# Kernel tuning notes

Measured on AMD Instinct MI355X. Metric: run time of the kernel, lower is better.

Reference implementation:

```python
import jax, jax.numpy as jnp
import numpy as np

H_IMG, W_IMG = 2160, 3840


def _avgpool3x3(x):
    # AvgPool2d(3, stride=1, padding=1), count_include_pad=True -> divide by 9 always
    s = jax.lax.reduce_window(x, 0.0, jax.lax.add, (3, 3, 1), (1, 1, 1), 'SAME')
    return s / 9.0


def setup_inputs() -> dict:
    key = jax.random.key(0)
    k1, k2, k3, k4 = jax.random.split(key, 4)
    depth = jax.random.uniform(k1, (H_IMG, W_IMG), jnp.float32) * 4.0 + 0.5
    rgb = jax.random.uniform(k2, (H_IMG, W_IMG, 3), jnp.float32)
    mask = jax.random.randint(k3, (H_IMG, W_IMG), 0, 2, jnp.int32)
    l = jax.random.normal(k4, (9, 3), jnp.float32) * 0.3
    fx = fy = 3000.0
    cx, cy = W_IMG / 2.0, H_IMG / 2.0
    CameraParam = jnp.array([[fx, 0.0, cx], [0.0, fy, cy], [0.0, 0.0, 1.0]], jnp.float32)
    return {'depth': depth, 'rgb': rgb, 'mask': mask, 'l': l, 'CameraParam': CameraParam}


def reference(depth, rgb, mask, l, CameraParam):
    nrows, ncols = depth.shape
    imask = mask > 0                      # [H, W] bool
    m3 = imask[..., None]                 # [H, W, 1]

    # Homogeneous pixel grid -> back-projected rays (precomputed in torch __init__)
    yy, xx = jnp.meshgrid(jnp.arange(nrows, dtype=jnp.float32),
                          jnp.arange(ncols, dtype=jnp.float32), indexing='ij')
    p2d = jnp.stack([xx, yy, jnp.ones_like(xx)], axis=-1)      # [H, W, 3]
    Kinv = jnp.linalg.inv(CameraParam)
    p3d = jnp.einsum('ij,hwj->hwi', Kinv, p2d)                 # [H, W, 3]

    # Depth -> 3D points, shifted neighbors (zero-padded at borders)
    p = p3d * depth[..., None]                                 # [H, W, 3]
    pl = jnp.pad(p[:, 1:, :], ((0, 0), (0, 1), (0, 0)))        # right neighbor
    pu = jnp.pad(p[1:, :, :], ((0, 1), (0, 0), (0, 0)))        # down neighbor

    n = jnp.cross(pl - p, pu - p)                              # [H, W, 3]
    norm = jnp.linalg.norm(n, axis=-1, keepdims=True)
    n = n / jnp.maximum(norm, 1e-12)                           # F.normalize

    nx, ny, nz = n[..., 0], n[..., 1], n[..., 2]
    ones = jnp.ones_like(nx)
    Hsh = jnp.stack([ones, ny, nz, nx, nx * ny, ny * nz,
                     -nx * nx - ny * ny + 2.0 * nz * nz,
                     nz * nx, nx * nx - ny * ny], axis=-1)     # [H, W, 9]
    B = jnp.einsum('hwk,kc->hwc', Hsh, l)                      # [H, W, 3]

    # Scatter into full image: zero outside mask (matches render_img[imask] = B)
    render = jnp.where(m3, B, 0.0)
    render_mean = jax.lax.stop_gradient(_avgpool3x3(render))   # render_img.detach()
    rgbmean = _avgpool3x3(jax.lax.stop_gradient(rgb))          # rgb.detach()

    diff = (render - render_mean) - (rgb - rgbmean)
    cnt = jnp.sum(imask).astype(jnp.float32) * 3.0             # MSE over masked elems
    loss = jnp.sum(jnp.where(m3, diff * diff, 0.0)) / cnt
    return loss
```

## Files before the change

### kernel.cpp

```cpp
#include <hip/hip_runtime.h>
#include <math.h>

#define H_IMG 2160
#define W_IMG 3840
#define SPAN 252
#define NSX 16
#define HS 12
#define WPB 4
#define NSY 45
#define NBLOCKS (NSX * NSY)
#define NBINS 2048

__global__ __launch_bounds__(256, 3) void shading_main(
    const float* __restrict__ depth,
    const float* __restrict__ rgb,
    const int*   __restrict__ mask,
    const float* __restrict__ lmat,
    const float* __restrict__ K,
    float* __restrict__ accum,
    int direct)
{
    const int tid  = threadIdx.x;
    const int lane = tid & 63;
    const int wv   = tid >> 6;
    const int sx   = blockIdx.x;
    const int x0   = sx * SPAN;
    const int y0   = blockIdx.y * (WPB * HS) + wv * HS;
    const int colBase = x0 + 4 * lane;
    const bool fullIn = (colBase + 3) < W_IMG;

    const float m00 = K[0], m01 = K[1], m02 = K[2];
    const float m10 = K[3], m11 = K[4], m12 = K[5];
    const float m20 = K[6], m21 = K[7], m22 = K[8];
    const float det = m00*(m11*m22 - m12*m21)
                    - m01*(m10*m22 - m12*m20)
                    + m02*(m10*m21 - m11*m20);
    const float id  = 1.0f / det;
    const float i00 = (m11*m22 - m12*m21) * id;
    const float i01 = (m02*m21 - m01*m22) * id;
    const float i02 = (m01*m12 - m02*m11) * id;
    const float i10 = (m12*m20 - m10*m22) * id;
    const float i11 = (m00*m22 - m02*m20) * id;
    const float i12 = (m02*m10 - m00*m12) * id;
    const float i20 = (m10*m21 - m11*m20) * id;
    const float i21 = (m01*m20 - m00*m21) * id;
    const float i22 = (m00*m11 - m01*m10) * id;

    float L[27];
    #pragma unroll
    for (int i = 0; i < 27; ++i) L[i] = lmat[i];

    float wout[4];
    #pragma unroll
    for (int k = 0; k < 4; ++k) {
        const int c  = colBase + k;
        const int lc = 4 * lane + k;
        const bool v = (c < W_IMG) && (lc <= SPAN) && (lc >= 1 || sx == 0);
        wout[k] = v ? 1.0f : 0.0f;
    }
    const float qm1s = (lane == 0) ? 0.0f : 1.0f;

    float rx = fmaf(i00, (float)colBase, fmaf(i01, (float)(y0 - 1), i02));
    float ry = fmaf(i10, (float)colBase, fmaf(i11, (float)(y0 - 1), i12));
    float rz = fmaf(i20, (float)colBase, fmaf(i21, (float)(y0 - 1), i22));

    const float4 Z4 = make_float4(0.f, 0.f, 0.f, 0.f);

    float4 dC = Z4, dN = Z4;
    float4 raC = Z4, rbC = Z4, rcC = Z4;
    int4   mC  = make_int4(0, 0, 0, 0);
    if (fullIn) {
        if (y0 > 0) {
            const long pix = (long)(y0 - 1) * W_IMG + colBase;
            dC  = *(const float4*)(depth + pix);
            raC = *(const float4*)(rgb + pix * 3);
            rbC = *(const float4*)(rgb + pix * 3 + 4);
            rcC = *(const float4*)(rgb + pix * 3 + 8);
            mC  = *(const int4*)(mask + pix);
        }
        dN = *(const float4*)(depth + (long)y0 * W_IMG + colBase);
    }

    float sA0[4] = {0,0,0,0}, sA1[4] = {0,0,0,0}, sA2[4] = {0,0,0,0};
    float sB0[4] = {0,0,0,0}, sB1[4] = {0,0,0,0}, sB2[4] = {0,0,0,0};
    float qB0[4] = {0,0,0,0}, qB1[4] = {0,0,0,0}, qB2[4] = {0,0,0,0};
    float wB[4]  = {0,0,0,0};
    float accS = 0.f, accC = 0.f;

    #pragma unroll 1
    for (int j = 0; j < HS + 2; ++j) {
        const int h = y0 - 1 + j;

        float4 dP = Z4, raN = Z4, rbN = Z4, rcN = Z4;
        int4   mN = make_int4(0, 0, 0, 0);
        if (fullIn) {
            if (h + 2 < H_IMG)
                dP = *(const float4*)(depth + (long)(h + 2) * W_IMG + colBase);
            if (h + 1 < H_IMG) {
                const long pix = (long)(h + 1) * W_IMG + colBase;
                raN = *(const float4*)(rgb + pix * 3);
                rbN = *(const float4*)(rgb + pix * 3 + 4);
                rcN = *(const float4*)(rgb + pix * 3 + 8);
                mN  = *(const int4*)(mask + pix);
            }
        }

        const float dcv[4] = {dC.x, dC.y, dC.z, dC.w};
        const float dnv[4] = {dN.x, dN.y, dN.z, dN.w};
        const float rrv[12] = {raC.x, raC.y, raC.z, raC.w,
                               rbC.x, rbC.y, rbC.z, rbC.w,
                               rcC.x, rcC.y, rcC.z, rcC.w};
        const int   mmv[4] = {mC.x, mC.y, mC.z, mC.w};
        const float dcR = __shfl_down(dC.x, 1, 64);

        float qC0[4], qC1[4], qC2[4], wC[4];
        float rxk = rx, ryk = ry, rzk = rz;
        #pragma unroll
        for (int k = 0; k < 4; ++k) {
            const float d0 = dcv[k];
            const float dR = (k < 3) ? dcv[k + 1] : dcR;
            const float dD = dnv[k];
            const float px = rxk * d0, py = ryk * d0, pz = rzk * d0;
            const float ax = (rxk + i00) * dR - px;
            const float ay = (ryk + i10) * dR - py;
            const float az = (rzk + i20) * dR - pz;
            const float bx = (rxk + i01) * dD - px;
            const float by = (ryk + i11) * dD - py;
            const float bz = (rzk + i21) * dD - pz;
            float nx = ay*bz - az*by;
            float ny = az*bx - ax*bz;
            float nz = ax*by - ay*bx;
            const float nn  = nx*nx + ny*ny + nz*nz;
            const float inr = __builtin_amdgcn_rsqf(fmaxf(nn, 1e-24f));
            nx *= inr; ny *= inr; nz *= inr;
            const float h4 = nx*ny, h5 = ny*nz, h7 = nz*nx;
            const float nx2 = nx*nx, ny2 = ny*ny, nz2 = nz*nz;
            const float h6 = 2.f*nz2 - nx2 - ny2;
            const float h8 = nx2 - ny2;
            const float B0 = L[0] + ny*L[3] + nz*L[6] + nx*L[9]  + h4*L[12] + h5*L[15] + h6*L[18] + h7*L[21] + h8*L[24];
            const float B1 = L[1] + ny*L[4] + nz*L[7] + nx*L[10] + h4*L[13] + h5*L[16] + h6*L[19] + h7*L[22] + h8*L[25];
            const float B2 = L[2] + ny*L[5] + nz*L[8] + nx*L[11] + h4*L[14] + h5*L[17] + h6*L[20] + h7*L[23] + h8*L[26];
            const float m  = (mmv[k] > 0) ? 1.0f : 0.0f;
            qC0[k] = fmaf(m, B0, -rrv[3*k + 0]);
            qC1[k] = fmaf(m, B1, -rrv[3*k + 1]);
            qC2[k] = fmaf(m, B2, -rrv[3*k + 2]);
            wC[k]  = m * wout[k];
            rxk += i00; ryk += i10; rzk += i20;
        }

        float sC0[4], sC1[4], sC2[4];
        {
            const float a0 = __shfl_up(qC0[3], 1, 64) * qm1s;
            const float a1 = __shfl_up(qC1[3], 1, 64) * qm1s;
            const float a2 = __shfl_up(qC2[3], 1, 64) * qm1s;
            const float p0 = __shfl_down(qC0[0], 1, 64);
            const float p1 = __shfl_down(qC1[0], 1, 64);
            const float p2 = __shfl_down(qC2[0], 1, 64);

            const float t01_0 = qC0[0] + qC0[1];
            const float t12_0 = qC0[1] + qC0[2];
            const float t23_0 = qC0[2] + qC0[3];
            sC0[0] = a0 + t01_0;
            sC0[1] = t01_0 + qC0[2];
            sC0[2] = t12_0 + qC0[3];
            sC0[3] = t23_0 + p0;

            const float t01_1 = qC1[0] + qC1[1];
            const float t12_1 = qC1[1] + qC1[2];
            const float t23_1 = qC1[2] + qC1[3];
            sC1[0] = a1 + t01_1;
            sC1[1] = t01_1 + qC1[2];
            sC1[2] = t12_1 + qC1[3];
            sC1[3] = t23_1 + p1;

            const float t01_2 = qC2[0] + qC2[1];
            const float t12_2 = qC2[1] + qC2[2];
            const float t23_2 = qC2[2] + qC2[3];
            sC2[0] = a2 + t01_2;
            sC2[1] = t01_2 + qC2[2];
            sC2[2] = t12_2 + qC2[3];
            sC2[3] = t23_2 + p2;
        }

        if (j >= 2) {
            #pragma unroll
            for (int k = 0; k < 4; ++k) {
                const float v0 = sA0[k] + sB0[k] + sC0[k];
                const float v1 = sA1[k] + sB1[k] + sC1[k];
                const float v2 = sA2[k] + sB2[k] + sC2[k];
                const float d0 = fmaf(v0, -(1.f/9.f), qB0[k]);
                const float d1 = fmaf(v1, -(1.f/9.f), qB1[k]);
                const float d2 = fmaf(v2, -(1.f/9.f), qB2[k]);
                const float w  = wB[k];
                accS = fmaf(w, d0*d0 + d1*d1 + d2*d2, accS);
                accC += w;
            }
        }

        #pragma unroll
        for (int k = 0; k < 4; ++k) {
            sA0[k] = sB0[k]; sA1[k] = sB1[k]; sA2[k] = sB2[k];
            sB0[k] = sC0[k]; sB1[k] = sC1[k]; sB2[k] = sC2[k];
            qB0[k] = qC0[k]; qB1[k] = qC1[k]; qB2[k] = qC2[k];
            wB[k]  = wC[k];
        }
        dC = dN; dN = dP;
        raC = raN; rbC = rbN; rcC = rcN; mC = mN;
        rx += i01; ry += i11; rz += i21;
    }

    #pragma unroll
    for (int off = 32; off > 0; off >>= 1) {
        accS += __shfl_down(accS, off, 64);
        accC += __shfl_down(accC, off, 64);
    }
    __shared__ float sS[WPB], sC[WPB];
    if (lane == 0) { sS[wv] = accS; sC[wv] = accC; }
    __syncthreads();
    if (tid == 0) {
        const float ts = sS[0] + sS[1] + sS[2] + sS[3];
        const float tc = sC[0] + sC[1] + sC[2] + sC[3];
        const int bid = blockIdx.y * gridDim.x + blockIdx.x;
        if (direct) {
            accum[2*bid + 0] = ts;
            accum[2*bid + 1] = tc;
        } else {
            const int bin = bid & (NBINS - 1);
            atomicAdd(&accum[2*bin + 0], ts);
            atomicAdd(&accum[2*bin + 1], tc);
        }
    }
}

__global__ __launch_bounds__(256) void finalize_kernel(
    const float* __restrict__ part, int n, float* __restrict__ out)
{
    const int tid = threadIdx.x;
    float s = 0.f, c = 0.f;
    for (int i = tid; i < n; i += 256) {
        s += part[2*i + 0];
        c += part[2*i + 1];
    }
    #pragma unroll
    for (int off = 32; off > 0; off >>= 1) {
        s += __shfl_down(s, off, 64);
        c += __shfl_down(c, off, 64);
    }
    __shared__ float sS[4], sC[4];
    const int wid = tid >> 6, lane = tid & 63;
    if (lane == 0) { sS[wid] = s; sC[wid] = c; }
    __syncthreads();
    if (tid == 0) {
        const float ts = sS[0] + sS[1] + sS[2] + sS[3];
        const float tc = sC[0] + sC[1] + sC[2] + sC[3];
        out[0] = ts / (3.0f * tc);
    }
}

extern "C" void kernel_launch(void* const* d_in, const int* in_sizes, int n_in,
                              void* d_out, int out_size, void* d_ws, size_t ws_size,
                              hipStream_t stream) {
    const float* depth = (const float*)d_in[0];
    const float* rgb   = (const float*)d_in[1];
    const int*   mask  = (const int*)  d_in[2];
    const float* lmat  = (const float*)d_in[3];
    const float* K     = (const float*)d_in[4];
    float* accum = (float*)d_ws;
    float* out   = (float*)d_out;

    const dim3 grid(NSX, NSY);

    if (ws_size >= (size_t)NBLOCKS * 2 * sizeof(float)) {
        shading_main<<<grid, 256, 0, stream>>>(depth, rgb, mask, lmat, K, accum, 1);
        finalize_kernel<<<1, 256, 0, stream>>>(accum, NBLOCKS, out);
    } else {
        hipMemsetAsync(accum, 0, NBINS * 2 * sizeof(float), stream);
        shading_main<<<grid, 256, 0, stream>>>(depth, rgb, mask, lmat, K, accum, 0);
        finalize_kernel<<<1, 256, 0, stream>>>(accum, NBINS, out);
    }
}
```

Measured before the change: 209.2 us.

## Shrink row strips to 8 rows and prefetch rgb/mask two rows ahead

Strips per wave go from 12 to 8 rows and blocks from 4 waves to 2, so the grid grows to 16x135 blocks of 128 threads. The rgb and mask loads now run two rows ahead instead of one, giving more time to hide memory latency, and loads past the strip end are skipped. The cost is more halo rows re-read per output row, more registers held for the deeper prefetch, and more partial sums for the finalize pass.

```diff
diff --git a/kernel.cpp b/kernel.cpp
--- a/kernel.cpp
+++ b/kernel.cpp
@@ -5,13 +5,13 @@
 #define W_IMG 3840
 #define SPAN 252
 #define NSX 16
-#define HS 12
-#define WPB 4
-#define NSY 45
+#define HS 8
+#define WPB 2
+#define NSY 135
 #define NBLOCKS (NSX * NSY)
 #define NBINS 2048
 
-__global__ __launch_bounds__(256, 3) void shading_main(
+__global__ __launch_bounds__(128, 4) void shading_main(
     const float* __restrict__ depth,
     const float* __restrict__ rgb,
     const int*   __restrict__ mask,
@@ -65,10 +65,12 @@
     float rz = fmaf(i20, (float)colBase, fmaf(i21, (float)(y0 - 1), i22));
 
     const float4 Z4 = make_float4(0.f, 0.f, 0.f, 0.f);
+    const int4  ZI4 = make_int4(0, 0, 0, 0);
 
     float4 dC = Z4, dN = Z4;
     float4 raC = Z4, rbC = Z4, rcC = Z4;
-    int4   mC  = make_int4(0, 0, 0, 0);
+    float4 raN1 = Z4, rbN1 = Z4, rcN1 = Z4;
+    int4   mC = ZI4, mN1 = ZI4;
     if (fullIn) {
         if (y0 > 0) {
             const long pix = (long)(y0 - 1) * W_IMG + colBase;
@@ -78,7 +80,14 @@
             rcC = *(const float4*)(rgb + pix * 3 + 8);
             mC  = *(const int4*)(mask + pix);
         }
-        dN = *(const float4*)(depth + (long)y0 * W_IMG + colBase);
+        {
+            const long pix = (long)y0 * W_IMG + colBase;
+            dN   = *(const float4*)(depth + pix);
+            raN1 = *(const float4*)(rgb + pix * 3);
+            rbN1 = *(const float4*)(rgb + pix * 3 + 4);
+            rcN1 = *(const float4*)(rgb + pix * 3 + 8);
+            mN1  = *(const int4*)(mask + pix);
+        }
     }
 
     float sA0[4] = {0,0,0,0}, sA1[4] = {0,0,0,0}, sA2[4] = {0,0,0,0};
@@ -91,17 +100,17 @@
     for (int j = 0; j < HS + 2; ++j) {
         const int h = y0 - 1 + j;
 
-        float4 dP = Z4, raN = Z4, rbN = Z4, rcN = Z4;
-        int4   mN = make_int4(0, 0, 0, 0);
-        if (fullIn) {
-            if (h + 2 < H_IMG)
-                dP = *(const float4*)(depth + (long)(h + 2) * W_IMG + colBase);
-            if (h + 1 < H_IMG) {
-                const long pix = (long)(h + 1) * W_IMG + colBase;
-                raN = *(const float4*)(rgb + pix * 3);
-                rbN = *(const float4*)(rgb + pix * 3 + 4);
-                rcN = *(const float4*)(rgb + pix * 3 + 8);
-                mN  = *(const int4*)(mask + pix);
+        float4 dP = Z4, raN2 = Z4, rbN2 = Z4, rcN2 = Z4;
+        int4   mN2 = ZI4;
+        if (fullIn && (h + 2) < H_IMG) {
+            const long pix = (long)(h + 2) * W_IMG + colBase;
+            if (j <= HS)
+                dP = *(const float4*)(depth + pix);
+            if (j < HS) {
+                raN2 = *(const float4*)(rgb + pix * 3);
+                rbN2 = *(const float4*)(rgb + pix * 3 + 4);
+                rcN2 = *(const float4*)(rgb + pix * 3 + 8);
+                mN2  = *(const int4*)(mask + pix);
             }
         }
 
@@ -205,7 +214,8 @@
             wB[k]  = wC[k];
         }
         dC = dN; dN = dP;
-        raC = raN; rbC = rbN; rcC = rcN; mC = mN;
+        raC = raN1; rbC = rbN1; rcC = rcN1; mC = mN1;
+        raN1 = raN2; rbN1 = rbN2; rcN1 = rcN2; mN1 = mN2;
         rx += i01; ry += i11; rz += i21;
     }
 
@@ -218,8 +228,8 @@
     if (lane == 0) { sS[wv] = accS; sC[wv] = accC; }
     __syncthreads();
     if (tid == 0) {
-        const float ts = sS[0] + sS[1] + sS[2] + sS[3];
-        const float tc = sC[0] + sC[1] + sC[2] + sC[3];
+        const float ts = sS[0] + sS[1];
+        const float tc = sC[0] + sC[1];
         const int bid = blockIdx.y * gridDim.x + blockIdx.x;
         if (direct) {
             accum[2*bid + 0] = ts;
@@ -271,11 +281,11 @@
     const dim3 grid(NSX, NSY);
 
     if (ws_size >= (size_t)NBLOCKS * 2 * sizeof(float)) {
-        shading_main<<<grid, 256, 0, stream>>>(depth, rgb, mask, lmat, K, accum, 1);
+        shading_main<<<grid, 128, 0, stream>>>(depth, rgb, mask, lmat, K, accum, 1);
         finalize_kernel<<<1, 256, 0, stream>>>(accum, NBLOCKS, out);
     } else {
         hipMemsetAsync(accum, 0, NBINS * 2 * sizeof(float), stream);
-        shading_main<<<grid, 256, 0, stream>>>(depth, rgb, mask, lmat, K, accum, 0);
+        shading_main<<<grid, 128, 0, stream>>>(depth, rgb, mask, lmat, K, accum, 0);
         finalize_kernel<<<1, 256, 0, stream>>>(accum, NBINS, out);
     }
 }
```

New measurement: 348.5 us. 66.6% more time.
